# Kernel tuning notes

Hardware: AMD Instinct MI355X
Metric: run time of the kernel (lower is better)

Reference implementation:

```python
import jax, jax.numpy as jnp
import numpy as np

NH, NKV, HD = 32, 8, 64
GROUPS = NH // NKV
NLAYERS, FREQ = 30, 3
NSLOTS = 1 + NLAYERS // FREQ  # 11
LAYER_IDX = 0
TOPK = 128
KB_SCALE = 100.0
PAD = -3.3895313892515355e+38  # torch.finfo(bfloat16).min


def rotate_half(x):
    d = x.shape[-1] // 2
    return jnp.concatenate([-x[..., d:], x[..., :d]], axis=-1)


def apply_rope(x, cos, sin):
    # x: (B, H, S, D); cos/sin: (B, S, D)
    return x * cos[:, None] + rotate_half(x) * sin[:, None]


def setup_inputs() -> dict:
    key = jax.random.key(0)
    ks = jax.random.split(key, 10)
    B, S, H = 2, 1024, 2048
    KBL = 400
    hidden_states = jax.random.normal(ks[0], (B, S, H), jnp.float32)
    # rotary embeddings (LlamaRotaryEmbedding, theta=10000)
    pos = jnp.arange(S, dtype=jnp.float32)
    inv_freq = 1.0 / (10000.0 ** (jnp.arange(0, HD, 2, dtype=jnp.float32) / HD))
    freqs = pos[:, None] * inv_freq[None, :]
    emb = jnp.concatenate([freqs, freqs], axis=-1)  # (S, HD)
    cos = jnp.broadcast_to(jnp.cos(emb)[None], (B, S, HD)).astype(jnp.float32)
    sin = jnp.broadcast_to(jnp.sin(emb)[None], (B, S, HD)).astype(jnp.float32)
    # additive causal mask (B,1,S,S)
    causal = jnp.where(jnp.tril(jnp.ones((S, S), jnp.bool_)), 0.0, PAD).astype(jnp.float32)
    attention_mask = jnp.broadcast_to(causal[None, None], (B, 1, S, S))
    kb_keys = jax.random.normal(ks[1], (KBL, NSLOTS * NH * HD), jnp.float32) * 0.5
    kb_values = jax.random.normal(ks[2], (KBL, NSLOTS * NH * HD), jnp.float32) * 0.5
    s = 0.02
    Wq = jax.random.normal(ks[3], (NH * HD, H), jnp.float32) * s
    Wq2 = jax.random.normal(ks[4], (NH * HD, H), jnp.float32) * s
    Wk = jax.random.normal(ks[5], (NKV * HD, H), jnp.float32) * s
    Wv = jax.random.normal(ks[6], (NKV * HD, H), jnp.float32) * s
    Wo = jax.random.normal(ks[7], (H, NH * HD), jnp.float32) * s
    return {"hidden_states": hidden_states, "cos": cos, "sin": sin,
            "attention_mask": attention_mask, "kb_keys": kb_keys, "kb_values": kb_values,
            "Wq": Wq, "Wq2": Wq2, "Wk": Wk, "Wv": Wv, "Wo": Wo}


def reference(hidden_states, cos, sin, attention_mask, kb_keys, kb_values, Wq, Wq2, Wk, Wv, Wo):
    B, S, H = hidden_states.shape
    scale = 1.0 / jnp.sqrt(jnp.float32(HD))

    # projections (attention_bias=False)
    q = (hidden_states @ Wq.T).reshape(B, S, NH, HD).transpose(0, 2, 1, 3)
    q2 = (hidden_states @ Wq2.T).reshape(B, S, NH, HD).transpose(0, 2, 1, 3)
    k = (hidden_states @ Wk.T).reshape(B, S, NKV, HD).transpose(0, 2, 1, 3)
    v = (hidden_states @ Wv.T).reshape(B, S, NKV, HD).transpose(0, 2, 1, 3)

    q = apply_rope(q, cos, sin)
    k = apply_rope(k, cos, sin)

    # repeat_kv (GQA)
    k = jnp.repeat(k, GROUPS, axis=1)  # (B, NH, S, HD)
    v = jnp.repeat(v, GROUPS, axis=1)

    # KB slot select (layer_idx % freq == 0, kb_idx = layer_idx // freq = 0)
    KBL = kb_keys.shape[0]
    kb_idx = LAYER_IDX // FREQ
    kbk = kb_keys.reshape(KBL, NSLOTS, NH * HD)[:, kb_idx].reshape(KBL, NH, HD).transpose(1, 0, 2)
    kbv = kb_values.reshape(KBL, NSLOTS, NH * HD)[:, kb_idx].reshape(KBL, NH, HD).transpose(1, 0, 2)
    kbk = jnp.broadcast_to(kbk[None], (B, NH, KBL, HD))
    kbv = jnp.broadcast_to(kbv[None], (B, NH, KBL, HD))

    # dynamic_sparsify: prune_key_value
    aw_kb = jnp.einsum('bhsd,bhkd->bhsk', q2, kbk) * scale  # (B,NH,S,KBL)
    scores = aw_kb.sum(axis=(1, 2))  # (B, KBL)
    top_idx = jax.lax.stop_gradient(jax.lax.top_k(scores, TOPK)[1])  # (B, TOPK)
    idx = jnp.broadcast_to(top_idx[:, None, :, None], (B, NH, TOPK, HD))
    kbk_g = jax.lax.stop_gradient(jnp.take_along_axis(kbk, idx, axis=2))  # gather under no_grad
    kbv_g = jax.lax.stop_gradient(jnp.take_along_axis(kbv, idx, axis=2))
    aw2 = aw_kb[..., :TOPK]  # source slices (not gathers) the first topk columns

    key_states = jnp.concatenate([kbk_g, k], axis=2)  # (B,NH,TOPK+S,HD)
    value_states = jnp.concatenate([kbv_g, v], axis=2)

    # KB attention mask block
    padding = jnp.all(attention_mask < 0, axis=-1, keepdims=True)  # (B,1,S,1)
    kb_mask = jnp.where(padding, PAD, 0.0).astype(attention_mask.dtype)
    kb_mask = jnp.broadcast_to(kb_mask, (B, 1, S, TOPK))
    mask = jnp.concatenate([kb_mask, attention_mask], axis=-1)  # (B,1,S,TOPK+S)

    aw = jnp.einsum('bhsd,bhkd->bhsk', q, key_states) * scale
    # seperate_query_head: replace KB block with q2-based scores (with kb scale shift)
    aw_seq = aw[..., TOPK:]
    aw2 = aw2 - np.log(TOPK) + np.log(KB_SCALE)
    aw = jnp.concatenate([aw2, aw_seq], axis=-1)

    aw = aw + mask[:, :, :, :key_states.shape[2]]
    aw = jax.nn.softmax(aw.astype(jnp.float32), axis=-1).astype(q.dtype)

    attn = jnp.einsum('bhsk,bhkd->bhsd', aw, value_states)  # (B,NH,S,HD)
    attn = attn.transpose(0, 2, 1, 3).reshape(B, S, NH * HD)
    return attn @ Wo.T
```

## Files before the change

kernel.cpp:

```cpp
#include <hip/hip_runtime.h>
#include <hip/hip_bf16.h>
#include <math.h>

#define NH 32
#define NKV 8
#define HD 64
#define NSLOTS 11
#define TOPK 128
#define KBROW (NSLOTS * NH * HD)
#define PADF (-3.3895313892515355e+38f)
#define C0F  (-0.24686007793152578f)
#define SCALE 0.125f
#define HCH 32

typedef __attribute__((ext_vector_type(8))) __bf16 bf16x8;
typedef __attribute__((ext_vector_type(8))) unsigned short u16x8;
typedef __attribute__((ext_vector_type(4))) float f32x4;

#define GLDS16(gp, lp)                                                        \
  __builtin_amdgcn_global_load_lds(                                           \
      (__attribute__((address_space(1))) void*)(gp),                          \
      (__attribute__((address_space(3))) void*)(lp), 16, 0, 0)

__device__ __forceinline__ unsigned short f2bf(float f) {
  unsigned int u = __float_as_uint(f);
  u = (u + 0x7fffu + ((u >> 16) & 1u)) >> 16;
  return (unsigned short)u;
}

__device__ __forceinline__ int swz(int row, int chunk) {
  return row * 128 + ((chunk ^ (row & 7)) << 4);
}

__global__ void f2bf_all(const float* __restrict__ s0, const float* __restrict__ s1,
                         const float* __restrict__ s2, const float* __restrict__ s3,
                         const float* __restrict__ s4,
                         int n0, int n1, int n2, int n3, int n4_,
                         unsigned short* __restrict__ out) {
  int i = blockIdx.x * blockDim.x + threadIdx.x;
  int j = i;
  const float* src;
  if (j < n0) src = s0;
  else { j -= n0; if (j < n1) src = s1;
  else { j -= n1; if (j < n2) src = s2;
  else { j -= n2; if (j < n3) src = s3;
  else { j -= n3; if (j >= n4_) return; src = s4; }}}}
  float4 v = ((const float4*)src)[j];
  ushort4 o = {f2bf(v.x), f2bf(v.y), f2bf(v.z), f2bf(v.w)};
  ((ushort4*)out)[i] = o;
}

__global__ __launch_bounds__(256) void gemm_nt_splitk(
    const unsigned short* __restrict__ A, const unsigned short* __restrict__ B,
    float* __restrict__ C0, float* __restrict__ C1, int M, int N, int K) {
  __shared__ unsigned short ldsA[128 * 32];
  __shared__ unsigned short ldsB[128 * 32];
  const int t = threadIdx.x;
  const int l = t & 63, w = t >> 6;
  const int wr = w >> 1, wc = w & 1;
  const int lr = l & 15;
  const int kb = (l >> 4) * 16;
  const int bm = blockIdx.y * 128, bn = blockIdx.x * 128;
  float* C = blockIdx.z ? C1 : C0;
  const int k0base = blockIdx.z * (K >> 1);
  const int kend = k0base + (K >> 1);

  f32x4 acc[4][4] = {};

  for (int k0 = k0base; k0 < kend; k0 += 32) {
    __syncthreads();
#pragma unroll
    for (int it = 0; it < 2; ++it) {
      int s = it * 256 + t;
      int row = s >> 2, cs = (s & 3) * 8;
      GLDS16(A + (size_t)(bm + row) * K + k0 + cs,
             (char*)ldsA + (it * 4 + w) * 1024);
      GLDS16(B + (size_t)(bn + row) * K + k0 + cs,
             (char*)ldsB + (it * 4 + w) * 1024);
    }
    __syncthreads();

    bf16x8 a[4], b[4];
#pragma unroll
    for (int m = 0; m < 4; ++m)
      a[m] = *(const bf16x8*)((const char*)ldsA +
                              (wr * 64 + m * 16 + lr) * 64 + kb);
#pragma unroll
    for (int n = 0; n < 4; ++n)
      b[n] = *(const bf16x8*)((const char*)ldsB +
                              (wc * 64 + n * 16 + lr) * 64 + kb);
#pragma unroll
    for (int m = 0; m < 4; ++m)
#pragma unroll
      for (int n = 0; n < 4; ++n)
        acc[m][n] =
            __builtin_amdgcn_mfma_f32_16x16x32_bf16(a[m], b[n], acc[m][n], 0, 0, 0);
  }

#pragma unroll
  for (int m = 0; m < 4; ++m)
#pragma unroll
    for (int n = 0; n < 4; ++n) {
      int rbase = bm + wr * 64 + m * 16 + ((l >> 4) << 2);
      int cbase = bn + wc * 64 + n * 16 + lr;
#pragma unroll
      for (int j = 0; j < 4; ++j)
        C[(size_t)(rbase + j) * N + cbase] = acc[m][n][j];
    }
}

__global__ void add2_kernel(const float* __restrict__ a,
                            const float* __restrict__ b,
                            float* __restrict__ o, int n4) {
  int i = blockIdx.x * blockDim.x + threadIdx.x;
  if (i >= n4) return;
  float4 x = ((const float4*)a)[i], y = ((const float4*)b)[i];
  ((float4*)o)[i] = make_float4(x.x + y.x, x.y + y.y, x.z + y.z, x.w + y.w);
}

__global__ __launch_bounds__(512) void gemm_proj8(
    const unsigned short* __restrict__ A,
    const unsigned short* __restrict__ Wall,
    const float* __restrict__ cosb, const float* __restrict__ sinb,
    unsigned short* __restrict__ qbf, unsigned short* __restrict__ q2bf,
    unsigned short* __restrict__ kbf, unsigned short* __restrict__ vTb,
    int M, int K, int S) {
  __shared__ char lds[131072];
  const int t = threadIdx.x;
  const int w = t >> 6;
  const int wm = w >> 2, wn = w & 3;
  const int l = t & 63;
  const int li = l & 15, lg4 = l >> 4;
  const int nwgx = gridDim.x;
  const int cpx = (nwgx * gridDim.y) >> 3;
  int linear = blockIdx.x + nwgx * blockIdx.y;
  int wid = (linear & 7) * cpx + (linear >> 3);
  const int bm = (wid / nwgx) * 256, bn = (wid % nwgx) * 256;
  const int NK = K >> 6;

  f32x4 acc[8][4] = {};

#define STAGE_UNIT(kt1, nb, u)                                                \
  {                                                                           \
    const int slice_ = (u) >> 1;                                              \
    const unsigned short* mat_ = ((u) & 1) ? Wall : A;                        \
    const int tb_ = ((u) & 1) ? bn : bm;                                      \
    char* base_ = lds + (nb) * 65536 + (((u) & 1) ? 32768 : 0) +              \
                  slice_ * 16384;                                             \
    _Pragma("unroll")                                                         \
    for (int i_ = 0; i_ < 2; ++i_) {                                          \
      int ss_ = i_ * 512 + t;                                                 \
      int row_ = ss_ >> 2, cc_ = ss_ & 3;                                     \
      int chunk_ = cc_ ^ ((row_ >> 1) & 3);                                   \
      GLDS16(mat_ + (size_t)(tb_ + row_) * K + (kt1) * 64 + slice_ * 32 +     \
                 chunk_ * 8,                                                  \
             base_ + i_ * 8192 + w * 1024);                                   \
    }                                                                         \
  }

  STAGE_UNIT(0, 0, 0); STAGE_UNIT(0, 0, 1);
  STAGE_UNIT(0, 0, 2); STAGE_UNIT(0, 0, 3);
  asm volatile("s_waitcnt vmcnt(4)" ::: "memory");
  asm volatile("s_barrier" ::: "memory");

  for (int kt = 0; kt < NK; ++kt) {
    const int cur = kt & 1;
    const bool stg = (kt + 1 < NK);
    char* curA = lds + cur * 65536;
    char* curB = curA + 32768;
#pragma unroll
    for (int kk = 0; kk < 2; ++kk) {
      bf16x8 bfr[4], af_a[4], af_b[4];
#pragma unroll
      for (int n = 0; n < 4; ++n) {
        int row = wn * 64 + n * 16 + li;
        bfr[n] = *(const bf16x8*)(curB + kk * 16384 + row * 64 +
                                  ((lg4 ^ ((row >> 1) & 3)) << 4));
      }
#pragma unroll
      for (int mi = 0; mi < 4; ++mi) {
        int row = wm * 128 + mi * 16 + li;
        af_a[mi] = *(const bf16x8*)(curA + kk * 16384 + row * 64 +
                                    ((lg4 ^ ((row >> 1) & 3)) << 4));
      }
      if (stg) STAGE_UNIT(kt + 1, cur ^ 1, kk * 2)
#pragma unroll
      for (int mi = 0; mi < 4; ++mi) {
        int row = wm * 128 + (4 + mi) * 16 + li;
        af_b[mi] = *(const bf16x8*)(curA + kk * 16384 + row * 64 +
                                    ((lg4 ^ ((row >> 1) & 3)) << 4));
      }
#pragma unroll
      for (int mi = 0; mi < 4; ++mi)
#pragma unroll
        for (int n = 0; n < 4; ++n)
          acc[mi][n] = __builtin_amdgcn_mfma_f32_16x16x32_bf16(
              af_a[mi], bfr[n], acc[mi][n], 0, 0, 0);
      if (stg) STAGE_UNIT(kt + 1, cur ^ 1, kk * 2 + 1)
#pragma unroll
      for (int mi = 0; mi < 4; ++mi)
#pragma unroll
        for (int n = 0; n < 4; ++n)
          acc[4 + mi][n] = __builtin_amdgcn_mfma_f32_16x16x32_bf16(
              af_b[mi], bfr[n], acc[4 + mi][n], 0, 0, 0);
      if (kk == 0) {
        if (kt == NK - 1) asm volatile("s_waitcnt vmcnt(0)" ::: "memory");
        else              asm volatile("s_waitcnt vmcnt(4)" ::: "memory");
        asm volatile("s_barrier" ::: "memory");
      } else {
        if (stg) {
          asm volatile("s_waitcnt vmcnt(4)" ::: "memory");
          asm volatile("s_barrier" ::: "memory");
        }
      }
    }
  }
#undef STAGE_UNIT

  const int seg = bn;
#pragma unroll
  for (int m = 0; m < 8; ++m) {
    const int row0 = bm + wm * 128 + m * 16 + lg4 * 4;
    if (seg < 2048 || (seg >= 4096 && seg < 4608)) {
      const bool isq = seg < 2048;
#pragma unroll
      for (int j = 0; j < 4; ++j) {
        int row = row0 + j;
        const float* cr = cosb + (size_t)row * 64;
        const float* sr = sinb + (size_t)row * 64;
        float c0 = cr[li], c1 = cr[16 + li], c2 = cr[32 + li], c3 = cr[48 + li];
        float sa = sr[li], sb = sr[16 + li], sc_ = sr[32 + li], sd = sr[48 + li];
        float x0 = acc[m][0][j], x1 = acc[m][1][j];
        float x2 = acc[m][2][j], x3 = acc[m][3][j];
        float y0 = x0 * c0 - x2 * sa;
        float y1 = x1 * c1 - x3 * sb;
        float y2 = x2 * c2 + x0 * sc_;
        float y3 = x3 * c3 + x1 * sd;
        if (isq) {
          size_t ro = (size_t)row * 2048 + bn + wn * 64 + li;
          qbf[ro] = f2bf(y0); qbf[ro + 16] = f2bf(y1);
          qbf[ro + 32] = f2bf(y2); qbf[ro + 48] = f2bf(y3);
        } else {
          size_t ro = (size_t)row * 512 + (bn - 4096) + wn * 64 + li;
          kbf[ro] = f2bf(y0); kbf[ro + 16] = f2bf(y1);
          kbf[ro + 32] = f2bf(y2); kbf[ro + 48] = f2bf(y3);
        }
      }
    } else if (seg < 4096) {
#pragma unroll
      for (int n = 0; n < 4; ++n) {
        int col = bn - 2048 + wn * 64 + n * 16 + li;
#pragma unroll
        for (int j = 0; j < 4; ++j)
          q2bf[(size_t)(row0 + j) * 2048 + col] = f2bf(acc[m][n][j]);
      }
    } else {
      int b_ = row0 / S, s = row0 % S;
#pragma unroll
      for (int n = 0; n < 4; ++n) {
        int col = (bn - 4608) + wn * 64 + n * 16 + li;
        int gg = col >> 6, d = col & 63;
        ushort4 o = {f2bf(acc[m][n][0]), f2bf(acc[m][n][1]),
                     f2bf(acc[m][n][2]), f2bf(acc[m][n][3])};
        *(ushort4*)&vTb[(((size_t)b_ * NKV + gg) * 64 + d) * S + s] = o;
      }
    }
  }
}

__global__ void kbkh_kernel(const float* __restrict__ kbk,
                            unsigned short* __restrict__ out) {
  int i = blockIdx.x * blockDim.x + threadIdx.x;
  if (i >= 128 * 512) return;
  int j = i >> 9, c4 = (i & 511) * 4;
  float4 v = *(const float4*)&kbk[(size_t)j * KBROW + c4];
  ushort4 o = {f2bf(v.x), f2bf(v.y), f2bf(v.z), f2bf(v.w)};
  *(ushort4*)&out[(size_t)j * 2048 + c4] = o;
}

__global__ __launch_bounds__(256) void kbvgt_kernel(
    const float* __restrict__ kbv, const int* __restrict__ topi,
    unsigned short* __restrict__ kbvgT, int B) {
  int h = blockIdx.x % NH, b = blockIdx.x / NH;
  __shared__ unsigned short gt[128][72];
  __shared__ int lidx[TOPK];
  int t = threadIdx.x;
  if (t < TOPK) lidx[t] = topi[b * TOPK + t];
  __syncthreads();
#pragma unroll
  for (int it = 0; it < 8; ++it) {
    int slot = it * 256 + t;
    int j = slot >> 4, d4 = (slot & 15) * 4;
    float4 v = *(const float4*)&kbv[(size_t)lidx[j] * KBROW + h * 64 + d4];
    gt[j][d4] = f2bf(v.x); gt[j][d4 + 1] = f2bf(v.y);
    gt[j][d4 + 2] = f2bf(v.z); gt[j][d4 + 3] = f2bf(v.w);
  }
  __syncthreads();
#pragma unroll
  for (int it = 0; it < 4; ++it) {
    int slot = it * 256 + t;
    int d = slot >> 4, j8 = (slot & 15) * 8;
    u16x8 o;
#pragma unroll
    for (int j = 0; j < 8; ++j) o[j] = gt[j8 + j][d];
    *(u16x8*)&kbvgT[(((size_t)b * NH + h) * 64 + d) * 128 + j8] = o;
  }
}

__global__ __launch_bounds__(256) void hsum1_kernel(
    const float* __restrict__ hidden, double* __restrict__ part,
    unsigned short* __restrict__ hbf, int B, int S, int H) {
  const int nhb = H >> 8;
  int hb = blockIdx.x % nhb;
  int ch = (blockIdx.x / nhb) % HCH;
  int b  = blockIdx.x / (nhb * HCH);
  int c  = hb * 256 + threadIdx.x;
  int rows = S / HCH;
  size_t base = ((size_t)b * S + (size_t)ch * rows) * H + c;
  const float* p = hidden + base;
  double acc = 0.0;
  for (int s = 0; s < rows; ++s) {
    float v = p[(size_t)s * H];
    acc += (double)v;
    hbf[base + (size_t)s * H] = f2bf(v);
  }
  part[((size_t)b * HCH + ch) * H + c] = acc;
}

__global__ void hsum2_kernel(const double* __restrict__ part,
                             float* __restrict__ Hsum, int B, int H) {
  int idx = blockIdx.x * blockDim.x + threadIdx.x;
  if (idx >= B * H) return;
  int b = idx / H, c = idx % H;
  const double* p = part + (size_t)b * HCH * H + c;
  double acc = 0.0;
#pragma unroll
  for (int ch = 0; ch < HCH; ++ch) acc += p[(size_t)ch * H];
  Hsum[idx] = (float)acc;
}

__global__ void qs_kernel(const float* __restrict__ Hsum,
                          const float* __restrict__ Wq2,
                          float* __restrict__ Qs, int B, int H) {
  int task = (blockIdx.x * blockDim.x + threadIdx.x) >> 6;
  int lane = threadIdx.x & 63;
  if (task >= B * NH * HD) return;
  int b = task / (NH * HD), c = task % (NH * HD);
  const float* hs = Hsum + (size_t)b * H;
  const float* wr = Wq2 + (size_t)c * H;
  double acc = 0.0;
  for (int k = lane; k < H; k += 64) acc += (double)hs[k] * (double)wr[k];
#pragma unroll
  for (int off = 32; off; off >>= 1) acc += __shfl_xor(acc, off);
  if (lane == 0) Qs[task] = (float)acc;
}

__global__ void scores_kernel(const float* __restrict__ Qs,
                              const float* __restrict__ kbk,
                              float* __restrict__ scores, int B, int KBL) {
  int task = (blockIdx.x * blockDim.x + threadIdx.x) >> 6;
  int lane = threadIdx.x & 63;
  if (task >= B * KBL) return;
  int b = task / KBL, l = task % KBL;
  const float* kr = kbk + (size_t)l * KBROW;
  const float* qd = Qs + (size_t)b * NH * HD;
  double acc = 0.0;
  for (int c = lane; c < NH * HD; c += 64) acc += (double)qd[c] * (double)kr[c];
#pragma unroll
  for (int off = 32; off; off >>= 1) acc += __shfl_xor(acc, off);
  if (lane == 0) scores[task] = (float)(0.125 * acc);
}

__global__ __launch_bounds__(256) void topk_kernel(
    const float* __restrict__ scores, int* __restrict__ top_idx, int KBL) {
  __shared__ float ls[512];
  int b = blockIdx.x, t = threadIdx.x;
  for (int i = t; i < KBL; i += 256) ls[i] = scores[(size_t)b * KBL + i];
  __syncthreads();
  for (int l = t; l < KBL; l += 256) {
    float sl = ls[l];
    int rank = 0;
    for (int j = 0; j < KBL; ++j) {
      float sj = ls[j];
      rank += (sj > sl || (sj == sl && j < l)) ? 1 : 0;
    }
    if (rank < TOPK) top_idx[b * TOPK + rank] = l;
  }
}

__global__ void padflag_kernel(const float* __restrict__ mask,
                               int* __restrict__ flags, int BS, int S) {
  int w = (blockIdx.x * blockDim.x + threadIdx.x) >> 6;
  int lane = threadIdx.x & 63;
  if (w >= BS) return;
  const float* row = mask + (size_t)w * S;
  bool ok = true;
  for (int j = lane; j < S; j += 64) ok = ok && (row[j] < 0.f);
  int allv = __all(ok ? 1 : 0);
  if (lane == 0) flags[w] = allv;
}

__device__ __forceinline__ void load_chunk(
    int ch, int t, int b, int h, int g, int S,
    const unsigned short* __restrict__ kbf, const unsigned short* __restrict__ vTb,
    const unsigned short* __restrict__ kbkh, const unsigned short* __restrict__ kbvgT,
    bf16x8* st) {
  bool iskb = ch < 2;
  int j0 = iskb ? ch * 64 : (ch - 2) * 64;
#pragma unroll
  for (int it = 0; it < 4; ++it) {
    int slot = it * 256 + t;
    int tile = slot >> 9, row = (slot >> 3) & 63, ck = slot & 7;
    const unsigned short* src;
    if (tile == 0)
      src = iskb ? kbkh + (size_t)(j0 + row) * 2048 + h * 64 + ck * 8
                 : kbf + (size_t)(b * S + j0 + row) * 512 + g * 64 + ck * 8;
    else
      src = iskb ? kbvgT + (((size_t)b * NH + h) * 64 + row) * 128 + j0 + ck * 8
                 : vTb + (((size_t)b * NKV + g) * 64 + row) * (size_t)S + j0 + ck * 8;
    st[it] = *(const bf16x8*)src;
  }
}

__device__ __forceinline__ void attn_step(
    const char* smem, char* ptw, const int* padfb, const bf16x8* aq,
    bool iskb, int j0, int s0, int w, int li, int lg4,
    float* m_, float* l_, f32x4* acc) {
  f32x4 cc[4];
  __builtin_amdgcn_s_setprio(1);
#pragma unroll
  for (int cb = 0; cb < 4; ++cb) {
    bf16x8 b0 = *(const bf16x8*)(smem + swz(cb * 16 + li, lg4));
    bf16x8 b1 = *(const bf16x8*)(smem + swz(cb * 16 + li, 4 + lg4));
    f32x4 z = {};
    z = __builtin_amdgcn_mfma_f32_16x16x32_bf16(aq[0], b0, z, 0, 0, 0);
    z = __builtin_amdgcn_mfma_f32_16x16x32_bf16(aq[1], b1, z, 0, 0, 0);
    cc[cb] = z;
  }
  __builtin_amdgcn_s_setprio(0);

  float lgv[4][4];
#pragma unroll
  for (int cb = 0; cb < 4; ++cb)
#pragma unroll
    for (int j = 0; j < 4; ++j) {
      float v = SCALE * cc[cb][j];
      if (iskb) {
        v += C0F + (padfb[w * 16 + lg4 * 4 + j] ? PADF : 0.f);
      } else {
        int key = j0 + cb * 16 + li;
        int srow = s0 + w * 16 + lg4 * 4 + j;
        v += (key <= srow) ? 0.f : PADF;
      }
      lgv[cb][j] = v;
    }
#pragma unroll
  for (int j = 0; j < 4; ++j) {
    float rmax = fmaxf(fmaxf(lgv[0][j], lgv[1][j]), fmaxf(lgv[2][j], lgv[3][j]));
#pragma unroll
    for (int off = 8; off; off >>= 1) rmax = fmaxf(rmax, __shfl_xor(rmax, off));
    float mn = fmaxf(m_[j], rmax);
    float fs = __expf(m_[j] - mn);
    float csum = 0.f;
#pragma unroll
    for (int cb = 0; cb < 4; ++cb) {
      float pv = __expf(lgv[cb][j] - mn);
      csum += pv;
      int key = cb * 16 + li;
      int rloc = lg4 * 4 + j;
      *(unsigned short*)(ptw + swz(rloc, key >> 3) + ((key & 7) << 1)) = f2bf(pv);
    }
#pragma unroll
    for (int off = 8; off; off >>= 1) csum += __shfl_xor(csum, off);
    m_[j] = mn;
    l_[j] = l_[j] * fs + csum;
#pragma unroll
    for (int db = 0; db < 4; ++db) acc[db][j] *= fs;
  }

  bf16x8 pa0 = *(const bf16x8*)(ptw + swz(li, lg4));
  bf16x8 pa1 = *(const bf16x8*)(ptw + swz(li, 4 + lg4));
  __builtin_amdgcn_s_setprio(1);
#pragma unroll
  for (int db = 0; db < 4; ++db) {
    bf16x8 bv0 = *(const bf16x8*)(smem + 8192 + swz(db * 16 + li, lg4));
    bf16x8 bv1 = *(const bf16x8*)(smem + 8192 + swz(db * 16 + li, 4 + lg4));
    acc[db] = __builtin_amdgcn_mfma_f32_16x16x32_bf16(pa0, bv0, acc[db], 0, 0, 0);
    acc[db] = __builtin_amdgcn_mfma_f32_16x16x32_bf16(pa1, bv1, acc[db], 0, 0, 0);
  }
  __builtin_amdgcn_s_setprio(0);
}

__global__ __launch_bounds__(256) void attn_mfma(
    const unsigned short* __restrict__ qbf,
    const unsigned short* __restrict__ q2bf,
    const unsigned short* __restrict__ kbf,
    const unsigned short* __restrict__ vTb,
    const unsigned short* __restrict__ kbkh,
    const unsigned short* __restrict__ kbvgT,
    const int* __restrict__ padflag,
    unsigned short* __restrict__ attnbf,
    int B, int S) {
  const int nst = S >> 6;
  const int npair = (nst + 1) >> 1;
  const int p = blockIdx.x % npair;
  const int h = (blockIdx.x / npair) % NH;
  const int b = blockIdx.x / (npair * NH);
  const int stA = p, stB = nst - 1 - p;
  const bool hasB = (stB != stA);
  const int s0A = stA * 64, s0B = stB * 64;
  const int g = h / (NH / NKV);

  __shared__ unsigned short smem[8192];
  __shared__ unsigned short pt[4][1024];
  __shared__ int padf[128];

  const int t = threadIdx.x;
  const int w = t >> 6;
  const int li = t & 15;
  const int lg4 = (t & 63) >> 4;

  const int nch = 2 + stB + 1;

  bf16x8 st[4];
  load_chunk(0, t, b, h, g, S, kbf, vTb, kbkh, kbvgT, st);

  bf16x8 aq0A[2], aq2A[2], aq0B[2], aq2B[2];
  {
    size_t rowA = (size_t)(b * S + s0A + w * 16 + li) * (NH * HD);
    size_t rowB = (size_t)(b * S + s0B + w * 16 + li) * (NH * HD);
#pragma unroll
    for (int kc = 0; kc < 2; ++kc) {
      size_t o = h * 64 + kc * 32 + lg4 * 8;
      aq0A[kc] = *(const bf16x8*)(qbf + rowA + o);
      aq2A[kc] = *(const bf16x8*)(q2bf + rowA + o);
      aq0B[kc] = *(const bf16x8*)(qbf + rowB + o);
      aq2B[kc] = *(const bf16x8*)(q2bf + rowB + o);
    }
  }
  if (t < 64) padf[t] = padflag[b * S + s0A + t];
  else if (t < 128) padf[t] = padflag[b * S + s0B + (t - 64)];

  float mA[4] = {-3.4e38f, -3.4e38f, -3.4e38f, -3.4e38f};
  float mB[4] = {-3.4e38f, -3.4e38f, -3.4e38f, -3.4e38f};
  float lA[4] = {}, lB[4] = {};
  f32x4 accA[4] = {}, accB[4] = {};

  for (int ch = 0; ch < nch; ++ch) {
    const bool iskb = ch < 2;
    const int j0 = iskb ? ch * 64 : (ch - 2) * 64;
    if (ch) __syncthreads();
#pragma unroll
    for (int it = 0; it < 4; ++it) {
      int slot = it * 256 + t;
      int tile = slot >> 9, row = (slot >> 3) & 63, ck = slot & 7;
      *(bf16x8*)((char*)smem + tile * 8192 + swz(row, ck)) = st[it];
    }
    __syncthreads();
    if (ch + 1 < nch) load_chunk(ch + 1, t, b, h, g, S, kbf, vTb, kbkh, kbvgT, st);

    if (iskb || (ch - 2) <= stA)
      attn_step((const char*)smem, (char*)pt[w], padf, iskb ? aq2A : aq0A,
                iskb, j0, s0A, w, li, lg4, mA, lA, accA);
    if (hasB)
      attn_step((const char*)smem, (char*)pt[w], padf + 64, iskb ? aq2B : aq0B,
                iskb, j0, s0B, w, li, lg4, mB, lB, accB);
  }

#pragma unroll
  for (int j = 0; j < 4; ++j) {
    float inv = 1.f / lA[j];
    size_t o = (size_t)(b * S + s0A + w * 16 + lg4 * 4 + j) * (NH * HD) + h * 64 + li;
#pragma unroll
    for (int db = 0; db < 4; ++db) attnbf[o + db * 16] = f2bf(accA[db][j] * inv);
  }
  if (hasB) {
#pragma unroll
    for (int j = 0; j < 4; ++j) {
      float inv = 1.f / lB[j];
      size_t o = (size_t)(b * S + s0B + w * 16 + lg4 * 4 + j) * (NH * HD) + h * 64 + li;
#pragma unroll
      for (int db = 0; db < 4; ++db) attnbf[o + db * 16] = f2bf(accB[db][j] * inv);
    }
  }
}

extern "C" void kernel_launch(void* const* d_in, const int* in_sizes, int n_in,
                              void* d_out, int out_size, void* d_ws, size_t ws_size,
                              hipStream_t stream) {
  const float* hidden = (const float*)d_in[0];
  const float* cosb   = (const float*)d_in[1];
  const float* sinb   = (const float*)d_in[2];
  const float* mask   = (const float*)d_in[3];
  const float* kbk    = (const float*)d_in[4];
  const float* kbv    = (const float*)d_in[5];
  const float* Wq     = (const float*)d_in[6];
  const float* Wq2    = (const float*)d_in[7];
  const float* Wk     = (const float*)d_in[8];
  const float* Wv     = (const float*)d_in[9];
  const float* Wo     = (const float*)d_in[10];
  float* out = (float*)d_out;

  const int H   = in_sizes[6] / (NH * HD);
  const int KBL = in_sizes[4] / KBROW;
  const long long BSll = (long long)in_sizes[0] / H;
  const int S = (int)((long long)in_sizes[3] / BSll);
  const int B = (int)(BSll / S);
  const int BS = B * S;
  const int NQ = NH * HD;
  const int NKVD = NKV * HD;
  const int NTOT = NQ + NQ + NKVD + NKVD;

  float* ws = (float*)d_ws;
  size_t off = 0;
  double* hpart = (double*)(ws + off); off += (size_t)B * HCH * H * 2;
  float* Hsum = ws + off; off += (size_t)B * H;
  float* Qs   = ws + off; off += (size_t)B * NQ;
  float* sc   = ws + off; off += (size_t)B * KBL;
  int* topi   = (int*)(ws + off); off += (size_t)B * TOPK;
  int* padfl  = (int*)(ws + off); off += (size_t)BS;
  unsigned short* hbf    = (unsigned short*)(ws + off); off += (size_t)BS * H / 2;
  unsigned short* wall   = (unsigned short*)(ws + off); off += (size_t)NTOT * H / 2;
  unsigned short* wobf   = (unsigned short*)(ws + off); off += (size_t)H * NQ / 2;
  unsigned short* attnbf = (unsigned short*)(ws + off); off += (size_t)BS * NQ / 2;
  unsigned short* qbf    = (unsigned short*)(ws + off); off += (size_t)BS * NQ / 2;
  unsigned short* q2bf   = (unsigned short*)(ws + off); off += (size_t)BS * NQ / 2;
  unsigned short* kbf    = (unsigned short*)(ws + off); off += (size_t)BS * NKVD / 2;
  unsigned short* vTb    = (unsigned short*)(ws + off); off += (size_t)BS * NKVD / 2;
  unsigned short* kbkh   = (unsigned short*)(ws + off); off += (size_t)128 * NQ / 2;
  unsigned short* kbvgT  = (unsigned short*)(ws + off); off += (size_t)B * NH * HD * TOPK / 2;
  float* c0 = (float*)qbf;
  float* c1 = (float*)wall;
  (void)ws_size; (void)n_in; (void)out_size;

  {
    int n1 = NQ * H / 4, n2 = NQ * H / 4;
    int n3 = NKVD * H / 4, n4_ = NKVD * H / 4, n5 = H * NQ / 4;
    int ntot = n1 + n2 + n3 + n4_ + n5;
    f2bf_all<<<(ntot + 255) / 256, 256, 0, stream>>>(
        Wq, Wq2, Wk, Wv, Wo, n1, n2, n3, n4_, n5, wall);
  }

  hsum1_kernel<<<B * HCH * (H / 256), 256, 0, stream>>>(hidden, hpart, hbf, B, S, H);

  gemm_proj8<<<dim3(NTOT / 256, BS / 256), 512, 0, stream>>>(
      hbf, wall, cosb, sinb, qbf, q2bf, kbf, vTb, BS, H, S);

  hsum2_kernel<<<(B * H + 255) / 256, 256, 0, stream>>>(hpart, Hsum, B, H);
  qs_kernel<<<(B * NQ * 64 + 255) / 256, 256, 0, stream>>>(Hsum, Wq2, Qs, B, H);
  scores_kernel<<<(B * KBL * 64 + 255) / 256, 256, 0, stream>>>(Qs, kbk, sc, B, KBL);
  topk_kernel<<<B, 256, 0, stream>>>(sc, topi, KBL);
  padflag_kernel<<<(BS * 64 + 255) / 256, 256, 0, stream>>>(mask, padfl, BS, S);

  kbkh_kernel<<<(128 * 512 + 255) / 256, 256, 0, stream>>>(kbk, kbkh);
  kbvgt_kernel<<<B * NH, 256, 0, stream>>>(kbv, topi, kbvgT, B);

  {
    int nst = S / 64;
    int npair = (nst + 1) / 2;
    attn_mfma<<<B * NH * npair, 256, 0, stream>>>(
        qbf, q2bf, kbf, vTb, kbkh, kbvgT, padfl, attnbf, B, S);
  }

  gemm_nt_splitk<<<dim3(H / 128, BS / 128, 2), 256, 0, stream>>>(
      attnbf, wobf, c0, c1, BS, H, NQ);
  add2_kernel<<<(BS * H / 4 + 255) / 256, 256, 0, stream>>>(c0, c1, out, BS * H / 4);
}
```

Baseline: 250.4 us.

## Double-buffer attention K/V LDS tiles and drop GEMM block swizzle

```diff
diff --git a/kernel.cpp b/kernel.cpp
--- a/kernel.cpp
+++ b/kernel.cpp
@@ -131,11 +131,7 @@
   const int wm = w >> 2, wn = w & 3;
   const int l = t & 63;
   const int li = l & 15, lg4 = l >> 4;
-  const int nwgx = gridDim.x;
-  const int cpx = (nwgx * gridDim.y) >> 3;
-  int linear = blockIdx.x + nwgx * blockIdx.y;
-  int wid = (linear & 7) * cpx + (linear >> 3);
-  const int bm = (wid / nwgx) * 256, bn = (wid % nwgx) * 256;
+  const int bm = blockIdx.y * 256, bn = blockIdx.x * 256;
   const int NK = K >> 6;
 
   f32x4 acc[8][4] = {};
@@ -423,15 +419,15 @@
 }
 
 __device__ __forceinline__ void attn_step(
-    const char* smem, char* ptw, const int* padfb, const bf16x8* aq,
+    const char* cbuf, char* ptw, const int* padfb, const bf16x8* aq,
     bool iskb, int j0, int s0, int w, int li, int lg4,
     float* m_, float* l_, f32x4* acc) {
   f32x4 cc[4];
   __builtin_amdgcn_s_setprio(1);
 #pragma unroll
   for (int cb = 0; cb < 4; ++cb) {
-    bf16x8 b0 = *(const bf16x8*)(smem + swz(cb * 16 + li, lg4));
-    bf16x8 b1 = *(const bf16x8*)(smem + swz(cb * 16 + li, 4 + lg4));
+    bf16x8 b0 = *(const bf16x8*)(cbuf + swz(cb * 16 + li, lg4));
+    bf16x8 b1 = *(const bf16x8*)(cbuf + swz(cb * 16 + li, 4 + lg4));
     f32x4 z = {};
     z = __builtin_amdgcn_mfma_f32_16x16x32_bf16(aq[0], b0, z, 0, 0, 0);
     z = __builtin_amdgcn_mfma_f32_16x16x32_bf16(aq[1], b1, z, 0, 0, 0);
@@ -483,8 +479,8 @@
   __builtin_amdgcn_s_setprio(1);
 #pragma unroll
   for (int db = 0; db < 4; ++db) {
-    bf16x8 bv0 = *(const bf16x8*)(smem + 8192 + swz(db * 16 + li, lg4));
-    bf16x8 bv1 = *(const bf16x8*)(smem + 8192 + swz(db * 16 + li, 4 + lg4));
+    bf16x8 bv0 = *(const bf16x8*)(cbuf + 8192 + swz(db * 16 + li, lg4));
+    bf16x8 bv1 = *(const bf16x8*)(cbuf + 8192 + swz(db * 16 + li, 4 + lg4));
     acc[db] = __builtin_amdgcn_mfma_f32_16x16x32_bf16(pa0, bv0, acc[db], 0, 0, 0);
     acc[db] = __builtin_amdgcn_mfma_f32_16x16x32_bf16(pa1, bv1, acc[db], 0, 0, 0);
   }
@@ -511,7 +507,7 @@
   const int s0A = stA * 64, s0B = stB * 64;
   const int g = h / (NH / NKV);
 
-  __shared__ unsigned short smem[8192];
+  __shared__ unsigned short smem[2][8192];
   __shared__ unsigned short pt[4][1024];
   __shared__ int padf[128];
 
@@ -541,6 +537,15 @@
   if (t < 64) padf[t] = padflag[b * S + s0A + t];
   else if (t < 128) padf[t] = padflag[b * S + s0B + (t - 64)];
 
+#pragma unroll
+  for (int it = 0; it < 4; ++it) {
+    int slot = it * 256 + t;
+    int tile = slot >> 9, row = (slot >> 3) & 63, ck = slot & 7;
+    *(bf16x8*)((char*)smem[0] + tile * 8192 + swz(row, ck)) = st[it];
+  }
+  load_chunk(1, t, b, h, g, S, kbf, vTb, kbkh, kbvgT, st);
+  __syncthreads();
+
   float mA[4] = {-3.4e38f, -3.4e38f, -3.4e38f, -3.4e38f};
   float mB[4] = {-3.4e38f, -3.4e38f, -3.4e38f, -3.4e38f};
   float lA[4] = {}, lB[4] = {};
@@ -549,22 +554,25 @@
   for (int ch = 0; ch < nch; ++ch) {
     const bool iskb = ch < 2;
     const int j0 = iskb ? ch * 64 : (ch - 2) * 64;
-    if (ch) __syncthreads();
-#pragma unroll
-    for (int it = 0; it < 4; ++it) {
-      int slot = it * 256 + t;
-      int tile = slot >> 9, row = (slot >> 3) & 63, ck = slot & 7;
-      *(bf16x8*)((char*)smem + tile * 8192 + swz(row, ck)) = st[it];
-    }
-    __syncthreads();
-    if (ch + 1 < nch) load_chunk(ch + 1, t, b, h, g, S, kbf, vTb, kbkh, kbvgT, st);
-
+    if (ch + 1 < nch) {
+      char* nb = (char*)smem[(ch + 1) & 1];
+#pragma unroll
+      for (int it = 0; it < 4; ++it) {
+        int slot = it * 256 + t;
+        int tile = slot >> 9, row = (slot >> 3) & 63, ck = slot & 7;
+        *(bf16x8*)(nb + tile * 8192 + swz(row, ck)) = st[it];
+      }
+      if (ch + 2 < nch)
+        load_chunk(ch + 2, t, b, h, g, S, kbf, vTb, kbkh, kbvgT, st);
+    }
+    const char* cb = (const char*)smem[ch & 1];
     if (iskb || (ch - 2) <= stA)
-      attn_step((const char*)smem, (char*)pt[w], padf, iskb ? aq2A : aq0A,
+      attn_step(cb, (char*)pt[w], padf, iskb ? aq2A : aq0A,
                 iskb, j0, s0A, w, li, lg4, mA, lA, accA);
     if (hasB)
-      attn_step((const char*)smem, (char*)pt[w], padf + 64, iskb ? aq2B : aq0B,
+      attn_step(cb, (char*)pt[w], padf + 64, iskb ? aq2B : aq0B,
                 iskb, j0, s0B, w, li, lg4, mB, lB, accB);
+    __syncthreads();
   }
 
 #pragma unroll
```

Measured after the change: 247.6 us. About the same (-1.1%).
